# Kernel optimization log

Measured on AMD Instinct MI355X. Metric: run time of the kernel, lower is better.

The kernel has to match this reference:

```python
import jax, jax.numpy as jnp
import numpy as np

N_NODES = 40000
N_EDGES = 320000
N_GRAPHS = 64
IN_DIM = 128
HID4 = 256   # hidden_dim * 4
OUT_DIM = 128
LN_EPS = 1e-5


def setup_inputs() -> dict:
    key = jax.random.key(0)
    ks = jax.random.split(key, 12)
    x = jax.random.normal(ks[0], (N_NODES, IN_DIM), dtype=jnp.float32)
    w = jax.random.uniform(ks[1], (N_EDGES, 4), dtype=jnp.float32)
    src = jax.random.randint(ks[2], (N_EDGES,), 0, N_NODES, dtype=jnp.int32)
    dst = jax.random.randint(ks[3], (N_EDGES,), 0, N_NODES, dtype=jnp.int32)
    graph_ids = jnp.sort(jax.random.randint(ks[4], (N_NODES,), 0, N_GRAPHS, dtype=jnp.int32))
    # parameters (no biases on GraphConv / fc1 linear)
    W1 = jax.random.normal(ks[5], (IN_DIM, HID4), dtype=jnp.float32) / np.sqrt(IN_DIM)
    fc1_W = jax.random.normal(ks[6], (IN_DIM, HID4), dtype=jnp.float32) / np.sqrt(IN_DIM)
    ln_gamma = jnp.ones((HID4,), dtype=jnp.float32)
    ln_beta = jnp.zeros((HID4,), dtype=jnp.float32)
    W2 = jax.random.normal(ks[7], (2 * HID4, HID4), dtype=jnp.float32) / np.sqrt(2 * HID4)
    W3 = jax.random.normal(ks[8], (HID4, OUT_DIM), dtype=jnp.float32) / np.sqrt(HID4)
    return {"x": x, "w": w, "W1": W1, "fc1_W": fc1_W, "ln_gamma": ln_gamma,
            "ln_beta": ln_beta, "W2": W2, "W3": W3,
            "src": src, "dst": dst, "graph_ids": graph_ids}


def _graph_conv(feat, src, dst, ew, W, out_inv_sqrt, in_inv_sqrt):
    # DGL GraphConv, norm='both', bias=False, with scalar edge_weight:
    # h = D_out^{-1/2} x ; m_e = w_e * h[src] ; agg = scatter_add(m, dst) ;
    # out = (D_in^{-1/2} agg) @ W
    h = feat * out_inv_sqrt[:, None]
    m = h[src] * ew[:, None]                       # [E, D] messages
    agg = jax.ops.segment_sum(m, dst, num_segments=N_NODES)
    return (agg * in_inv_sqrt[:, None]) @ W


def reference(x, w, W1, fc1_W, ln_gamma, ln_beta, W2, W3, src, dst, graph_ids):
    # unweighted degree normalization (DGL uses structural degrees, clamp(min=1))
    ones_e = jnp.ones((N_EDGES,), dtype=x.dtype)
    out_deg = jnp.maximum(jax.ops.segment_sum(ones_e, src, num_segments=N_NODES), 1.0)
    in_deg = jnp.maximum(jax.ops.segment_sum(ones_e, dst, num_segments=N_NODES), 1.0)
    out_inv = out_deg ** -0.5
    in_inv = in_deg ** -0.5

    ew = jnp.max(w, axis=1)                        # [E]

    x1 = jax.nn.relu(_graph_conv(x, src, dst, ew, W1, out_inv, in_inv))

    # fc1: Linear(no bias) -> LayerNorm(affine) -> ReLU
    f1 = x @ fc1_W
    mu = jnp.mean(f1, axis=-1, keepdims=True)
    var = jnp.mean((f1 - mu) ** 2, axis=-1, keepdims=True)
    f1 = (f1 - mu) * jax.lax.rsqrt(var + LN_EPS) * ln_gamma + ln_beta
    f1 = jax.nn.relu(f1)

    x1f1 = jnp.concatenate([x1, f1], axis=1)       # [N, 512]
    x2 = jax.nn.relu(_graph_conv(x1f1, src, dst, ew, W2, out_inv, in_inv))
    x3 = jax.nn.relu(_graph_conv(x2, src, dst, ew, W3, out_inv, in_inv))

    # dgl.sum_nodes over batched graph, then row-wise L2 normalize
    readout = jax.ops.segment_sum(x3, graph_ids, num_segments=N_GRAPHS)  # [G, OUT_DIM]
    norm = jnp.maximum(jnp.linalg.norm(readout, axis=1, keepdims=True), 1e-12)
    return readout / norm
```

## Files before the change

### kernel.cpp

```cpp
#include <hip/hip_runtime.h>

#define N_NODES 40000
#define M_PAD   40064
#define N_EDGES 320000
#define N_GRAPHS 64
#define IN_DIM 128
#define HID4 256
#define OUT_DIM 128
#define LN_EPS 1e-5f

typedef short  s16x8  __attribute__((ext_vector_type(8)));
typedef __bf16 bf16x8 __attribute__((ext_vector_type(8)));
typedef float  f32x4  __attribute__((ext_vector_type(4)));

__device__ __forceinline__ unsigned short f2b(float f) {
    unsigned int u = __builtin_bit_cast(unsigned int, f);
    u += 0x7fffu + ((u >> 16) & 1u);
    return (unsigned short)(u >> 16);
}
__device__ __forceinline__ float b2f(unsigned short h) {
    unsigned int u = (unsigned int)h << 16;
    return __builtin_bit_cast(float, u);
}

__device__ __forceinline__ void gll16(const unsigned short* g, short* lds_base) {
    __builtin_amdgcn_global_load_lds(
        (const __attribute__((address_space(1))) unsigned int*)g,
        (__attribute__((address_space(3))) unsigned int*)lds_base, 16, 0, 0);
}


#define XN (N_NODES * IN_DIM)
#define WN 229376
#define PREP_TOT (XN + WN + N_EDGES)

__global__ void prep_all(const float* __restrict__ x, const float* __restrict__ W1,
                         const float* __restrict__ fc1, const float* __restrict__ W2,
                         const float* __restrict__ W3, const float* __restrict__ w,
                         const int* __restrict__ src, const int* __restrict__ dst,
                         unsigned short* __restrict__ xb, unsigned short* __restrict__ W1t,
                         unsigned short* __restrict__ fc1t, unsigned short* __restrict__ W2t,
                         unsigned short* __restrict__ W3t, float* __restrict__ ew,
                         int* __restrict__ cnt_out, int* __restrict__ cnt_in) {
    int idx = blockIdx.x * 256 + threadIdx.x;
    if (idx < XN) { xb[idx] = f2b(x[idx]); return; }
    int j = idx - XN;
    if (j < 32768) { int k = j >> 8, n = j & 255; W1t[n * 128 + k] = f2b(W1[j]); return; }
    j -= 32768;
    if (j < 32768) { int k = j >> 8, n = j & 255; fc1t[n * 128 + k] = f2b(fc1[j]); return; }
    j -= 32768;
    if (j < 131072) { int k = j >> 8, n = j & 255; W2t[n * 512 + k] = f2b(W2[j]); return; }
    j -= 131072;
    if (j < 32768) { int k = j >> 7, n = j & 127; W3t[n * 256 + k] = f2b(W3[j]); return; }
    j -= 32768;
    if (j < N_EDGES) {
        float4 v = ((const float4*)w)[j];
        ew[j] = fmaxf(fmaxf(v.x, v.y), fmaxf(v.z, v.w));
        atomicAdd(&cnt_out[src[j]], 1);
        atomicAdd(&cnt_in[dst[j]], 1);
    }
}

__global__ void scan_part(const int* __restrict__ cnt, int* __restrict__ partial) {
    int b = blockIdx.x;
    int s = 0;
    for (int i = threadIdx.x; i < 1000; i += 256) s += cnt[b * 1000 + i];
#pragma unroll
    for (int m = 1; m < 64; m <<= 1) s += __shfl_xor(s, m);
    __shared__ int wsm[4];
    if ((threadIdx.x & 63) == 0) wsm[threadIdx.x >> 6] = s;
    __syncthreads();
    if (threadIdx.x == 0) partial[b] = wsm[0] + wsm[1] + wsm[2] + wsm[3];
}

__global__ void scan_final(const int* __restrict__ cnt_in, const int* __restrict__ cnt_out,
                           const int* __restrict__ partial, int* __restrict__ off,
                           float* __restrict__ out_inv, float* __restrict__ in_inv) {
    int b = blockIdx.x, tid = threadIdx.x;
    int lane = tid & 63, wv = tid >> 6;
    int pre = 0;
    for (int j = 0; j < b; ++j) pre += partial[j];
    int i = b * 1000 + tid;
    int v = (tid < 1000) ? cnt_in[i] : 0;
    int x = v;
#pragma unroll
    for (int ofs = 1; ofs < 64; ofs <<= 1) {
        int t = __shfl_up(x, ofs);
        if (lane >= ofs) x += t;
    }
    __shared__ int wsum[16];
    if (lane == 63) wsum[wv] = x;
    __syncthreads();
    if (wv == 0 && lane < 16) {
        int s = wsum[lane];
#pragma unroll
        for (int ofs = 1; ofs < 16; ofs <<= 1) {
            int t = __shfl_up(s, ofs);
            if (lane >= ofs) s += t;
        }
        wsum[lane] = s;
    }
    __syncthreads();
    int incl = pre + (wv > 0 ? wsum[wv - 1] : 0) + x;
    if (tid < 1000) {
        off[i] = incl - v;
        in_inv[i] = rsqrtf(fmaxf((float)v, 1.0f));
        out_inv[i] = rsqrtf(fmaxf((float)cnt_out[i], 1.0f));
    }
    if (b == 39 && tid == 999) off[N_NODES] = incl;
}

__global__ void csr_fill(const int* __restrict__ src, const int* __restrict__ dst,
                         const float* __restrict__ ew, const float* __restrict__ out_inv,
                         const int* __restrict__ off, int* __restrict__ cnt_in,
                         int2* __restrict__ es1, int2* __restrict__ es23) {
    int e = blockIdx.x * 256 + threadIdx.x;
    if (e >= N_EDGES) return;
    int d = dst[e];
    int slot = off[d] + atomicSub(&cnt_in[d], 1) - 1;
    int s = src[e];
    float wv = ew[e];
    es1[slot] = make_int2(s, __float_as_int(wv * out_inv[s]));
    es23[slot] = make_int2(s, __float_as_int(wv));
}


template <int D, int RELU>
__global__ void gather_nodes(const unsigned short* __restrict__ h, const int* __restrict__ off,
                             const int2* __restrict__ eg, const float* __restrict__ scale,
                             unsigned short* __restrict__ outb) {
    int n = blockIdx.x;
    int t = threadIdx.x;
    int b = off[n], e = off[n + 1];
    const unsigned int* hu = (const unsigned int*)h;
    float a0 = 0.0f, a1 = 0.0f;
    int i = b;
    for (; i + 3 < e; i += 4) {
        int2 e0 = eg[i], e1 = eg[i + 1], e2 = eg[i + 2], e3 = eg[i + 3];
        unsigned int p0 = hu[(size_t)e0.x * (D / 2) + t];
        unsigned int p1 = hu[(size_t)e1.x * (D / 2) + t];
        unsigned int p2 = hu[(size_t)e2.x * (D / 2) + t];
        unsigned int p3 = hu[(size_t)e3.x * (D / 2) + t];
        float w0 = __int_as_float(e0.y), w1 = __int_as_float(e1.y);
        float w2 = __int_as_float(e2.y), w3 = __int_as_float(e3.y);
        a0 += w0 * b2f((unsigned short)p0) + w1 * b2f((unsigned short)p1)
            + w2 * b2f((unsigned short)p2) + w3 * b2f((unsigned short)p3);
        a1 += w0 * b2f((unsigned short)(p0 >> 16)) + w1 * b2f((unsigned short)(p1 >> 16))
            + w2 * b2f((unsigned short)(p2 >> 16)) + w3 * b2f((unsigned short)(p3 >> 16));
    }
    for (; i < e; ++i) {
        int2 ee = eg[i];
        unsigned int p = hu[(size_t)ee.x * (D / 2) + t];
        float w0 = __int_as_float(ee.y);
        a0 += w0 * b2f((unsigned short)p);
        a1 += w0 * b2f((unsigned short)(p >> 16));
    }
    float sc = scale[n];
    a0 *= sc; a1 *= sc;
    if (RELU) { a0 = fmaxf(a0, 0.0f); a1 = fmaxf(a1, 0.0f); }
    unsigned int o = (unsigned int)f2b(a0) | ((unsigned int)f2b(a1) << 16);
    ((unsigned int*)outb)[(size_t)n * (D / 2) + t] = o;
}


#define G3_NPB 8

__global__ void gather3_ro(const unsigned short* __restrict__ h, const int* __restrict__ off,
                           const int2* __restrict__ eg, const float* __restrict__ scale,
                           const int* __restrict__ gid, float* __restrict__ ro) {
    int t = threadIdx.x;
    int n0 = blockIdx.x * G3_NPB;
    int n1 = n0 + G3_NPB;
    if (n1 > N_NODES) n1 = N_NODES;
    const unsigned int* hu = (const unsigned int*)h;
    float r0 = 0.0f, r1 = 0.0f;
    int cur = gid[n0];
    for (int n = n0; n < n1; ++n) {
        int g = gid[n];
        if (g != cur) {
            atomicAdd(&ro[cur * OUT_DIM + 2 * t], r0);
            atomicAdd(&ro[cur * OUT_DIM + 2 * t + 1], r1);
            r0 = r1 = 0.0f;
            cur = g;
        }
        int b = off[n], e = off[n + 1];
        float a0 = 0.0f, a1 = 0.0f;
        int i = b;
        for (; i + 3 < e; i += 4) {
            int2 e0 = eg[i], e1 = eg[i + 1], e2 = eg[i + 2], e3 = eg[i + 3];
            unsigned int p0 = hu[(size_t)e0.x * 64 + t];
            unsigned int p1 = hu[(size_t)e1.x * 64 + t];
            unsigned int p2 = hu[(size_t)e2.x * 64 + t];
            unsigned int p3 = hu[(size_t)e3.x * 64 + t];
            float w0 = __int_as_float(e0.y), w1 = __int_as_float(e1.y);
            float w2 = __int_as_float(e2.y), w3 = __int_as_float(e3.y);
            a0 += w0 * b2f((unsigned short)p0) + w1 * b2f((unsigned short)p1)
                + w2 * b2f((unsigned short)p2) + w3 * b2f((unsigned short)p3);
            a1 += w0 * b2f((unsigned short)(p0 >> 16)) + w1 * b2f((unsigned short)(p1 >> 16))
                + w2 * b2f((unsigned short)(p2 >> 16)) + w3 * b2f((unsigned short)(p3 >> 16));
        }
        for (; i < e; ++i) {
            int2 ee = eg[i];
            unsigned int p = hu[(size_t)ee.x * 64 + t];
            float w0 = __int_as_float(ee.y);
            a0 += w0 * b2f((unsigned short)p);
            a1 += w0 * b2f((unsigned short)(p >> 16));
        }
        float sc = scale[n];
        r0 += fmaxf(a0 * sc, 0.0f);
        r1 += fmaxf(a1 * sc, 0.0f);
    }
    atomicAdd(&ro[cur * OUT_DIM + 2 * t], r0);
    atomicAdd(&ro[cur * OUT_DIM + 2 * t + 1], r1);
}


__device__ __forceinline__ void gemm_core(short* As, short* Bs,
    const unsigned short* __restrict__ A, const unsigned short* __restrict__ A2,
    const unsigned short* __restrict__ Bt, unsigned short* __restrict__ C,
    const float* __restrict__ rowScaleC, int K1, int K2, int N,
    int relu, int scaleC, int m0, int n0) {
    int tid = threadIdx.x;
    int lane = tid & 63, wave = tid >> 6;
    int wm = (wave >> 1) * 64, wn = (wave & 1) * 64;
    int quad = lane >> 4, r16 = lane & 15;
    const int K = K1 + K2;
    f32x4 acc[4][4] = {};
    int lrow = wave * 16 + (lane >> 2);
    int kc = (lane & 3) * 8;
    short* ldsA = As + wave * 512;
    short* ldsB = Bs + wave * 512;

    for (int k0 = 0; k0 < K; k0 += 32) {
        int kk = k0 + kc;
#pragma unroll
        for (int h = 0; h < 2; ++h) {
            int r = h * 64 + lrow;
            const unsigned short* Ap = (kk < K1)
                ? A  + (size_t)(m0 + r) * K1 + kk
                : A2 + (size_t)(m0 + r) * K2 + (kk - K1);
            gll16(Ap, ldsA + h * 2048);
            gll16(Bt + (size_t)(n0 + r) * K + kk, ldsB + h * 2048);
        }
        __syncthreads();
        s16x8 af[4], bfr[4];
#pragma unroll
        for (int i = 0; i < 4; ++i)
            af[i] = *(const s16x8*)(As + (wm + i * 16 + r16) * 32 + quad * 8);
#pragma unroll
        for (int j = 0; j < 4; ++j)
            bfr[j] = *(const s16x8*)(Bs + (wn + j * 16 + r16) * 32 + quad * 8);
#pragma unroll
        for (int i = 0; i < 4; ++i)
#pragma unroll
            for (int j = 0; j < 4; ++j)
                acc[i][j] = __builtin_amdgcn_mfma_f32_16x16x32_bf16(
                    __builtin_bit_cast(bf16x8, af[i]), __builtin_bit_cast(bf16x8, bfr[j]),
                    acc[i][j], 0, 0, 0);
        __syncthreads();
    }

#pragma unroll
    for (int i = 0; i < 4; ++i) {
        int mbase = m0 + wm + i * 16 + quad * 4;
#pragma unroll
        for (int r = 0; r < 4; ++r) {
            int m = mbase + r;
            float sc = scaleC ? rowScaleC[m] : 1.0f;
#pragma unroll
            for (int j = 0; j < 4; ++j) {
                float v = acc[i][j][r] * sc;
                if (relu) v = fmaxf(v, 0.0f);
                C[(size_t)m * N + n0 + wn + j * 16 + r16] = f2b(v);
            }
        }
    }
}

template <int RELU, int SCALE_C>
__global__ __launch_bounds__(256) void gemm_mfma(
    const unsigned short* __restrict__ A, const unsigned short* __restrict__ A2,
    const unsigned short* __restrict__ Bt, unsigned short* __restrict__ C,
    const float* __restrict__ rowScaleC, int K1, int K2, int N) {
    __shared__ short As[4096];
    __shared__ short Bs[4096];
    gemm_core(As, Bs, A, A2, Bt, C, rowScaleC, K1, K2, N, RELU, SCALE_C,
              blockIdx.x * 128, blockIdx.y * 128);
}


__global__ __launch_bounds__(512) void gemm_dual(
    const unsigned short* __restrict__ A0, const unsigned short* __restrict__ B0,
    unsigned short* __restrict__ C0,
    const unsigned short* __restrict__ A1, const unsigned short* __restrict__ B1,
    unsigned short* __restrict__ C1,
    const float* __restrict__ gamma, const float* __restrict__ beta) {
    __shared__ short As[4096];
    __shared__ short Bs[8192];
    __shared__ float lns[128][4];
    __shared__ float lnq[128][4];
    const unsigned short* A  = blockIdx.z ? A1 : A0;
    const unsigned short* Bt = blockIdx.z ? B1 : B0;
    unsigned short* C        = blockIdx.z ? C1 : C0;
    int tid = threadIdx.x;
    int lane = tid & 63, wave = tid >> 6;
    int wm = (wave >> 2) * 64, wn = (wave & 3) * 64;
    int quad = lane >> 4, r16 = lane & 15;
    int m0 = blockIdx.x * 128;
    f32x4 acc[4][4] = {};
    int lrow = lane >> 2;
    int kc = (lane & 3) * 8;
    short* ldsA = As + wave * 512;
    short* ldsB = Bs + wave * 512;

    for (int k0 = 0; k0 < 128; k0 += 32) {
        int kk = k0 + kc;
        int rr = wave * 16 + lrow;
        gll16(A + (size_t)(m0 + rr) * 128 + kk, ldsA);
        gll16(Bt + (size_t)rr * 128 + kk, ldsB);
        gll16(Bt + (size_t)(128 + rr) * 128 + kk, ldsB + 4096);
        __syncthreads();
        s16x8 af[4], bfr[4];
#pragma unroll
        for (int i = 0; i < 4; ++i)
            af[i] = *(const s16x8*)(As + (wm + i * 16 + r16) * 32 + quad * 8);
#pragma unroll
        for (int j = 0; j < 4; ++j)
            bfr[j] = *(const s16x8*)(Bs + (wn + j * 16 + r16) * 32 + quad * 8);
#pragma unroll
        for (int i = 0; i < 4; ++i)
#pragma unroll
            for (int j = 0; j < 4; ++j)
                acc[i][j] = __builtin_amdgcn_mfma_f32_16x16x32_bf16(
                    __builtin_bit_cast(bf16x8, af[i]), __builtin_bit_cast(bf16x8, bfr[j]),
                    acc[i][j], 0, 0, 0);
        __syncthreads();
    }

    if (blockIdx.z == 0) {
#pragma unroll
        for (int i = 0; i < 4; ++i) {
            int mbase = m0 + wm + i * 16 + quad * 4;
#pragma unroll
            for (int r = 0; r < 4; ++r) {
                int m = mbase + r;
#pragma unroll
                for (int j = 0; j < 4; ++j)
                    C[(size_t)m * 256 + wn + j * 16 + r16] = f2b(fmaxf(acc[i][j][r], 0.0f));
            }
        }
    } else {
#pragma unroll
        for (int i = 0; i < 4; ++i)
#pragma unroll
            for (int r = 0; r < 4; ++r) {
                float s = 0.0f, q = 0.0f;
#pragma unroll
                for (int j = 0; j < 4; ++j) { float v = acc[i][j][r]; s += v; q += v * v; }
#pragma unroll
                for (int m = 1; m < 16; m <<= 1) { s += __shfl_xor(s, m); q += __shfl_xor(q, m); }
                if (r16 == 0) {
                    int row = wm + i * 16 + quad * 4 + r;
                    lns[row][wave & 3] = s;
                    lnq[row][wave & 3] = q;
                }
            }
        __syncthreads();
#pragma unroll
        for (int i = 0; i < 4; ++i) {
#pragma unroll
            for (int r = 0; r < 4; ++r) {
                int row = wm + i * 16 + quad * 4 + r;
                float s = lns[row][0] + lns[row][1] + lns[row][2] + lns[row][3];
                float q = lnq[row][0] + lnq[row][1] + lnq[row][2] + lnq[row][3];
                float mu = s * (1.0f / HID4);
                float var = q * (1.0f / HID4) - mu * mu;
                float rs = rsqrtf(var + LN_EPS);
                int m = m0 + row;
#pragma unroll
                for (int j = 0; j < 4; ++j) {
                    int col = wn + j * 16 + r16;
                    float v = (acc[i][j][r] - mu) * rs * gamma[col] + beta[col];
                    C[(size_t)m * 256 + col] = f2b(fmaxf(v, 0.0f));
                }
            }
        }
    }
}


__global__ void normalize_out(const float* __restrict__ ro, float* __restrict__ out) {
    int g = blockIdx.x;
    int d = threadIdx.x;
    float v = ro[g * OUT_DIM + d];
    float ss = v * v;
#pragma unroll
    for (int m = 1; m < 64; m <<= 1) ss += __shfl_xor(ss, m);
    __shared__ float s2[2];
    if ((d & 63) == 0) s2[d >> 6] = ss;
    __syncthreads();
    float tot = s2[0] + s2[1];
    float norm = fmaxf(sqrtf(tot), 1e-12f);
    out[g * OUT_DIM + d] = v / norm;
}


extern "C" void kernel_launch(void* const* d_in, const int* in_sizes, int n_in,
                              void* d_out, int out_size, void* d_ws, size_t ws_size,
                              hipStream_t stream) {
    const float* x    = (const float*)d_in[0];
    const float* w    = (const float*)d_in[1];
    const float* W1   = (const float*)d_in[2];
    const float* fc1W = (const float*)d_in[3];
    const float* gam  = (const float*)d_in[4];
    const float* bet  = (const float*)d_in[5];
    const float* W2   = (const float*)d_in[6];
    const float* W3   = (const float*)d_in[7];
    const int* src = (const int*)d_in[8];
    const int* dst = (const int*)d_in[9];
    const int* gid = (const int*)d_in[10];
    float* out = (float*)d_out;

    float* ws = (float*)d_ws;
    float* out_inv = ws + 0;
    float* in_inv  = ws + 40000;
    float* ew      = ws + 80000;
    int*   cnt_out = (int*)(ws + 400000);
    int*   cnt_in  = (int*)(ws + 440000);
    float* ro      = ws + 480000;
    unsigned short* W1t  = (unsigned short*)(ws + 488192);
    unsigned short* fc1t = (unsigned short*)(ws + 504576);
    unsigned short* W2t  = (unsigned short*)(ws + 520960);
    unsigned short* W3t  = (unsigned short*)(ws + 586496);
    int*   partial = (int*)(ws + 602880);
    int*   off     = (int*)(ws + 602920);
    int2*  es1     = (int2*)(ws + 642922);
    int2*  es23    = (int2*)(ws + 1282922);
    unsigned short* xb    = (unsigned short*)(ws + 1923000);
    unsigned short* Q3b   = xb;
    unsigned short* agg1b = (unsigned short*)(ws + 4487100);
    unsigned short* x2b   = agg1b;
    unsigned short* x1b   = (unsigned short*)(ws + 9615300);
    unsigned short* f1b   = (unsigned short*)(ws + 14743500);
    unsigned short* P2b   = (unsigned short*)(ws + 19871700);

    hipMemsetAsync(cnt_out, 0, (2 * 40000 + N_GRAPHS * OUT_DIM) * sizeof(float), stream);

    prep_all<<<(PREP_TOT + 255) / 256, 256, 0, stream>>>(x, W1, fc1W, W2, W3, w, src, dst,
                                                         xb, W1t, fc1t, W2t, W3t, ew,
                                                         cnt_out, cnt_in);
    scan_part<<<40, 256, 0, stream>>>(cnt_in, partial);
    scan_final<<<40, 1024, 0, stream>>>(cnt_in, cnt_out, partial, off, out_inv, in_inv);
    csr_fill<<<(N_EDGES + 255) / 256, 256, 0, stream>>>(src, dst, ew, out_inv, off, cnt_in,
                                                        es1, es23);

    gather_nodes<IN_DIM, 0><<<N_NODES, IN_DIM / 2, 0, stream>>>(xb, off, es1, in_inv, agg1b);
    {
        dim3 grid(M_PAD / 128, 1, 2);
        gemm_dual<<<grid, 512, 0, stream>>>(agg1b, W1t, x1b, xb, fc1t, f1b, gam, bet);
    }

    {
        dim3 grid(M_PAD / 128, HID4 / 128);
        gemm_mfma<0, 1><<<grid, 256, 0, stream>>>(x1b, f1b, W2t, P2b, out_inv,
                                                  HID4, HID4, HID4);
    }
    gather_nodes<HID4, 1><<<N_NODES, HID4 / 2, 0, stream>>>(P2b, off, es23, in_inv, x2b);

    {
        dim3 grid(M_PAD / 128, OUT_DIM / 128);
        gemm_mfma<0, 1><<<grid, 256, 0, stream>>>(x2b, nullptr, W3t, Q3b, out_inv,
                                                  HID4, 0, OUT_DIM);
    }
    gather3_ro<<<(N_NODES + G3_NPB - 1) / G3_NPB, 64, 0, stream>>>(Q3b, off, es23, in_inv,
                                                                   gid, ro);
    normalize_out<<<N_GRAPHS, 128, 0, stream>>>(ro, out);
}
```

Measured before the change: 287.5 us.

## Merge edge arrays, widen gather loads, and use BK=64 swizzled LDS GEMM tiles

The two CSR edge arrays are merged into one int4 record holding source, normalized weight and raw weight. The gather kernels now use 64-lane blocks with 8-byte loads per lane. For 128-wide features, the two half-waves handle alternate edges and their sums are combined with a shuffle. The GEMM core moves to a K-step of 64 with an XOR-swizzled LDS layout and doubled shared memory, to cut bank conflicts and barrier count at the cost of more LDS per block (lower occupancy).

Measured after the change: 285.0 us. No clear change (-0.9%).

```diff
diff --git a/kernel.cpp b/kernel.cpp
--- a/kernel.cpp
+++ b/kernel.cpp
@@ -21,6 +21,11 @@
 __device__ __forceinline__ float b2f(unsigned short h) {
     unsigned int u = (unsigned int)h << 16;
     return __builtin_bit_cast(float, u);
+}
+__device__ __forceinline__ float lo2f(unsigned int u) { return b2f((unsigned short)u); }
+__device__ __forceinline__ float hi2f(unsigned int u) { return b2f((unsigned short)(u >> 16)); }
+__device__ __forceinline__ unsigned int packb(float x, float y) {
+    return (unsigned int)f2b(x) | ((unsigned int)f2b(y) << 16);
 }
 
 __device__ __forceinline__ void gll16(const unsigned short* g, short* lds_base) {
@@ -113,105 +118,150 @@
 __global__ void csr_fill(const int* __restrict__ src, const int* __restrict__ dst,
                          const float* __restrict__ ew, const float* __restrict__ out_inv,
                          const int* __restrict__ off, int* __restrict__ cnt_in,
-                         int2* __restrict__ es1, int2* __restrict__ es23) {
+                         int4* __restrict__ es) {
     int e = blockIdx.x * 256 + threadIdx.x;
     if (e >= N_EDGES) return;
     int d = dst[e];
     int slot = off[d] + atomicSub(&cnt_in[d], 1) - 1;
     int s = src[e];
     float wv = ew[e];
-    es1[slot] = make_int2(s, __float_as_int(wv * out_inv[s]));
-    es23[slot] = make_int2(s, __float_as_int(wv));
-}
-
-
-template <int D, int RELU>
+    es[slot] = make_int4(s, __float_as_int(wv * out_inv[s]), __float_as_int(wv), 0);
+}
+
+
+template <int D, int RELU, int WSEL>
 __global__ void gather_nodes(const unsigned short* __restrict__ h, const int* __restrict__ off,
-                             const int2* __restrict__ eg, const float* __restrict__ scale,
+                             const int4* __restrict__ eg, const float* __restrict__ scale,
                              unsigned short* __restrict__ outb) {
     int n = blockIdx.x;
-    int t = threadIdx.x;
+    int lane = threadIdx.x;
     int b = off[n], e = off[n + 1];
-    const unsigned int* hu = (const unsigned int*)h;
-    float a0 = 0.0f, a1 = 0.0f;
-    int i = b;
-    for (; i + 3 < e; i += 4) {
-        int2 e0 = eg[i], e1 = eg[i + 1], e2 = eg[i + 2], e3 = eg[i + 3];
-        unsigned int p0 = hu[(size_t)e0.x * (D / 2) + t];
-        unsigned int p1 = hu[(size_t)e1.x * (D / 2) + t];
-        unsigned int p2 = hu[(size_t)e2.x * (D / 2) + t];
-        unsigned int p3 = hu[(size_t)e3.x * (D / 2) + t];
-        float w0 = __int_as_float(e0.y), w1 = __int_as_float(e1.y);
-        float w2 = __int_as_float(e2.y), w3 = __int_as_float(e3.y);
-        a0 += w0 * b2f((unsigned short)p0) + w1 * b2f((unsigned short)p1)
-            + w2 * b2f((unsigned short)p2) + w3 * b2f((unsigned short)p3);
-        a1 += w0 * b2f((unsigned short)(p0 >> 16)) + w1 * b2f((unsigned short)(p1 >> 16))
-            + w2 * b2f((unsigned short)(p2 >> 16)) + w3 * b2f((unsigned short)(p3 >> 16));
-    }
-    for (; i < e; ++i) {
-        int2 ee = eg[i];
-        unsigned int p = hu[(size_t)ee.x * (D / 2) + t];
-        float w0 = __int_as_float(ee.y);
-        a0 += w0 * b2f((unsigned short)p);
-        a1 += w0 * b2f((unsigned short)(p >> 16));
-    }
-    float sc = scale[n];
-    a0 *= sc; a1 *= sc;
-    if (RELU) { a0 = fmaxf(a0, 0.0f); a1 = fmaxf(a1, 0.0f); }
-    unsigned int o = (unsigned int)f2b(a0) | ((unsigned int)f2b(a1) << 16);
-    ((unsigned int*)outb)[(size_t)n * (D / 2) + t] = o;
+    const uint2* hu = (const uint2*)h;
+    float a0 = 0.f, a1 = 0.f, a2 = 0.f, a3 = 0.f;
+    if constexpr (D == 256) {
+        int i = b;
+        for (; i + 3 < e; i += 4) {
+            int4 e0 = eg[i], e1 = eg[i + 1], e2 = eg[i + 2], e3 = eg[i + 3];
+            uint2 p0 = hu[(size_t)e0.x * 64 + lane];
+            uint2 p1 = hu[(size_t)e1.x * 64 + lane];
+            uint2 p2 = hu[(size_t)e2.x * 64 + lane];
+            uint2 p3 = hu[(size_t)e3.x * 64 + lane];
+            float w0 = __int_as_float(WSEL ? e0.z : e0.y);
+            float w1 = __int_as_float(WSEL ? e1.z : e1.y);
+            float w2 = __int_as_float(WSEL ? e2.z : e2.y);
+            float w3 = __int_as_float(WSEL ? e3.z : e3.y);
+            a0 += w0 * lo2f(p0.x) + w1 * lo2f(p1.x) + w2 * lo2f(p2.x) + w3 * lo2f(p3.x);
+            a1 += w0 * hi2f(p0.x) + w1 * hi2f(p1.x) + w2 * hi2f(p2.x) + w3 * hi2f(p3.x);
+            a2 += w0 * lo2f(p0.y) + w1 * lo2f(p1.y) + w2 * lo2f(p2.y) + w3 * lo2f(p3.y);
+            a3 += w0 * hi2f(p0.y) + w1 * hi2f(p1.y) + w2 * hi2f(p2.y) + w3 * hi2f(p3.y);
+        }
+        for (; i < e; ++i) {
+            int4 ee = eg[i];
+            uint2 p = hu[(size_t)ee.x * 64 + lane];
+            float w0 = __int_as_float(WSEL ? ee.z : ee.y);
+            a0 += w0 * lo2f(p.x); a1 += w0 * hi2f(p.x);
+            a2 += w0 * lo2f(p.y); a3 += w0 * hi2f(p.y);
+        }
+        float sc = scale[n];
+        a0 *= sc; a1 *= sc; a2 *= sc; a3 *= sc;
+        if (RELU) {
+            a0 = fmaxf(a0, 0.f); a1 = fmaxf(a1, 0.f);
+            a2 = fmaxf(a2, 0.f); a3 = fmaxf(a3, 0.f);
+        }
+        uint2 o; o.x = packb(a0, a1); o.y = packb(a2, a3);
+        ((uint2*)outb)[(size_t)n * 64 + lane] = o;
+    } else {
+        int half = lane >> 5, cl = lane & 31;
+        int i = b;
+        for (; i + 3 < e; i += 4) {
+            int4 ea = eg[i + half];
+            int4 eb = eg[i + 2 + half];
+            uint2 pa = hu[(size_t)ea.x * 32 + cl];
+            uint2 pb = hu[(size_t)eb.x * 32 + cl];
+            float wa = __int_as_float(WSEL ? ea.z : ea.y);
+            float wb = __int_as_float(WSEL ? eb.z : eb.y);
+            a0 += wa * lo2f(pa.x) + wb * lo2f(pb.x);
+            a1 += wa * hi2f(pa.x) + wb * hi2f(pb.x);
+            a2 += wa * lo2f(pa.y) + wb * lo2f(pb.y);
+            a3 += wa * hi2f(pa.y) + wb * hi2f(pb.y);
+        }
+        for (; i < e; i += 2) {
+            int idx = i + half;
+            int4 ee = eg[idx < e ? idx : i];
+            float w = (idx < e) ? __int_as_float(WSEL ? ee.z : ee.y) : 0.0f;
+            uint2 p = hu[(size_t)ee.x * 32 + cl];
+            a0 += w * lo2f(p.x); a1 += w * hi2f(p.x);
+            a2 += w * lo2f(p.y); a3 += w * hi2f(p.y);
+        }
+        a0 += __shfl_xor(a0, 32); a1 += __shfl_xor(a1, 32);
+        a2 += __shfl_xor(a2, 32); a3 += __shfl_xor(a3, 32);
+        float sc = scale[n];
+        a0 *= sc; a1 *= sc; a2 *= sc; a3 *= sc;
+        if (RELU) {
+            a0 = fmaxf(a0, 0.f); a1 = fmaxf(a1, 0.f);
+            a2 = fmaxf(a2, 0.f); a3 = fmaxf(a3, 0.f);
+        }
+        if (half == 0) {
+            uint2 o; o.x = packb(a0, a1); o.y = packb(a2, a3);
+            ((uint2*)outb)[(size_t)n * 32 + cl] = o;
+        }
+    }
 }
 
 
 #define G3_NPB 8
 
 __global__ void gather3_ro(const unsigned short* __restrict__ h, const int* __restrict__ off,
-                           const int2* __restrict__ eg, const float* __restrict__ scale,
+                           const int4* __restrict__ eg, const float* __restrict__ scale,
                            const int* __restrict__ gid, float* __restrict__ ro) {
-    int t = threadIdx.x;
+    int lane = threadIdx.x;
+    int half = lane >> 5, cl = lane & 31;
     int n0 = blockIdx.x * G3_NPB;
     int n1 = n0 + G3_NPB;
     if (n1 > N_NODES) n1 = N_NODES;
-    const unsigned int* hu = (const unsigned int*)h;
-    float r0 = 0.0f, r1 = 0.0f;
+    const uint2* hu = (const uint2*)h;
+    float r0 = 0.f, r1 = 0.f, r2 = 0.f, r3 = 0.f;
     int cur = gid[n0];
     for (int n = n0; n < n1; ++n) {
         int g = gid[n];
         if (g != cur) {
-            atomicAdd(&ro[cur * OUT_DIM + 2 * t], r0);
-            atomicAdd(&ro[cur * OUT_DIM + 2 * t + 1], r1);
-            r0 = r1 = 0.0f;
+            atomicAdd(&ro[cur * OUT_DIM + 4 * cl + 2 * half], half ? r2 : r0);
+            atomicAdd(&ro[cur * OUT_DIM + 4 * cl + 2 * half + 1], half ? r3 : r1);
+            r0 = r1 = r2 = r3 = 0.f;
             cur = g;
         }
         int b = off[n], e = off[n + 1];
-        float a0 = 0.0f, a1 = 0.0f;
+        float a0 = 0.f, a1 = 0.f, a2 = 0.f, a3 = 0.f;
         int i = b;
         for (; i + 3 < e; i += 4) {
-            int2 e0 = eg[i], e1 = eg[i + 1], e2 = eg[i + 2], e3 = eg[i + 3];
-            unsigned int p0 = hu[(size_t)e0.x * 64 + t];
-            unsigned int p1 = hu[(size_t)e1.x * 64 + t];
-            unsigned int p2 = hu[(size_t)e2.x * 64 + t];
-            unsigned int p3 = hu[(size_t)e3.x * 64 + t];
-            float w0 = __int_as_float(e0.y), w1 = __int_as_float(e1.y);
-            float w2 = __int_as_float(e2.y), w3 = __int_as_float(e3.y);
-            a0 += w0 * b2f((unsigned short)p0) + w1 * b2f((unsigned short)p1)
-                + w2 * b2f((unsigned short)p2) + w3 * b2f((unsigned short)p3);
-            a1 += w0 * b2f((unsigned short)(p0 >> 16)) + w1 * b2f((unsigned short)(p1 >> 16))
-                + w2 * b2f((unsigned short)(p2 >> 16)) + w3 * b2f((unsigned short)(p3 >> 16));
-        }
-        for (; i < e; ++i) {
-            int2 ee = eg[i];
-            unsigned int p = hu[(size_t)ee.x * 64 + t];
-            float w0 = __int_as_float(ee.y);
-            a0 += w0 * b2f((unsigned short)p);
-            a1 += w0 * b2f((unsigned short)(p >> 16));
-        }
+            int4 ea = eg[i + half];
+            int4 eb = eg[i + 2 + half];
+            uint2 pa = hu[(size_t)ea.x * 32 + cl];
+            uint2 pb = hu[(size_t)eb.x * 32 + cl];
+            float wa = __int_as_float(ea.z), wb = __int_as_float(eb.z);
+            a0 += wa * lo2f(pa.x) + wb * lo2f(pb.x);
+            a1 += wa * hi2f(pa.x) + wb * hi2f(pb.x);
+            a2 += wa * lo2f(pa.y) + wb * lo2f(pb.y);
+            a3 += wa * hi2f(pa.y) + wb * hi2f(pb.y);
+        }
+        for (; i < e; i += 2) {
+            int idx = i + half;
+            int4 ee = eg[idx < e ? idx : i];
+            float w = (idx < e) ? __int_as_float(ee.z) : 0.0f;
+            uint2 p = hu[(size_t)ee.x * 32 + cl];
+            a0 += w * lo2f(p.x); a1 += w * hi2f(p.x);
+            a2 += w * lo2f(p.y); a3 += w * hi2f(p.y);
+        }
+        a0 += __shfl_xor(a0, 32); a1 += __shfl_xor(a1, 32);
+        a2 += __shfl_xor(a2, 32); a3 += __shfl_xor(a3, 32);
         float sc = scale[n];
         r0 += fmaxf(a0 * sc, 0.0f);
         r1 += fmaxf(a1 * sc, 0.0f);
-    }
-    atomicAdd(&ro[cur * OUT_DIM + 2 * t], r0);
-    atomicAdd(&ro[cur * OUT_DIM + 2 * t + 1], r1);
+        r2 += fmaxf(a2 * sc, 0.0f);
+        r3 += fmaxf(a3 * sc, 0.0f);
+    }
+    atomicAdd(&ro[cur * OUT_DIM + 4 * cl + 2 * half], half ? r2 : r0);
+    atomicAdd(&ro[cur * OUT_DIM + 4 * cl + 2 * half + 1], half ? r3 : r1);
 }
 
 
@@ -226,37 +276,42 @@
     int quad = lane >> 4, r16 = lane & 15;
     const int K = K1 + K2;
     f32x4 acc[4][4] = {};
-    int lrow = wave * 16 + (lane >> 2);
-    int kc = (lane & 3) * 8;
-    short* ldsA = As + wave * 512;
-    short* ldsB = Bs + wave * 512;
-
-    for (int k0 = 0; k0 < K; k0 += 32) {
-        int kk = k0 + kc;
-#pragma unroll
-        for (int h = 0; h < 2; ++h) {
-            int r = h * 64 + lrow;
-            const unsigned short* Ap = (kk < K1)
+    int srow = lane >> 3;
+    int sk   = ((lane & 7) ^ srow) * 8;
+    int xorc = r16 & 7;
+    short* ldsA = As + wave * 2048;
+    short* ldsB = Bs + wave * 2048;
+
+    for (int k0 = 0; k0 < K; k0 += 64) {
+        int kk = k0 + sk;
+#pragma unroll
+        for (int h = 0; h < 4; ++h) {
+            int r = wave * 32 + h * 8 + srow;
+            const unsigned short* Ap = (k0 < K1)
                 ? A  + (size_t)(m0 + r) * K1 + kk
                 : A2 + (size_t)(m0 + r) * K2 + (kk - K1);
-            gll16(Ap, ldsA + h * 2048);
-            gll16(Bt + (size_t)(n0 + r) * K + kk, ldsB + h * 2048);
+            gll16(Ap, ldsA + h * 512);
+            gll16(Bt + (size_t)(n0 + r) * K + kk, ldsB + h * 512);
         }
         __syncthreads();
-        s16x8 af[4], bfr[4];
-#pragma unroll
-        for (int i = 0; i < 4; ++i)
-            af[i] = *(const s16x8*)(As + (wm + i * 16 + r16) * 32 + quad * 8);
-#pragma unroll
-        for (int j = 0; j < 4; ++j)
-            bfr[j] = *(const s16x8*)(Bs + (wn + j * 16 + r16) * 32 + quad * 8);
-#pragma unroll
-        for (int i = 0; i < 4; ++i)
+#pragma unroll
+        for (int c = 0; c < 2; ++c) {
+            s16x8 af[4], bfr[4];
+            int pc = (((c * 4 + quad) ^ xorc) << 3);
+#pragma unroll
+            for (int i = 0; i < 4; ++i)
+                af[i] = *(const s16x8*)(As + (wm + i * 16 + r16) * 64 + pc);
 #pragma unroll
             for (int j = 0; j < 4; ++j)
-                acc[i][j] = __builtin_amdgcn_mfma_f32_16x16x32_bf16(
-                    __builtin_bit_cast(bf16x8, af[i]), __builtin_bit_cast(bf16x8, bfr[j]),
-                    acc[i][j], 0, 0, 0);
+                bfr[j] = *(const s16x8*)(Bs + (wn + j * 16 + r16) * 64 + pc);
+#pragma unroll
+            for (int i = 0; i < 4; ++i)
+#pragma unroll
+                for (int j = 0; j < 4; ++j)
+                    acc[i][j] = __builtin_amdgcn_mfma_f32_16x16x32_bf16(
+                        __builtin_bit_cast(bf16x8, af[i]), __builtin_bit_cast(bf16x8, bfr[j]),
+                        acc[i][j], 0, 0, 0);
+        }
         __syncthreads();
     }
 
@@ -282,8 +337,8 @@
     const unsigned short* __restrict__ A, const unsigned short* __restrict__ A2,
     const unsigned short* __restrict__ Bt, unsigned short* __restrict__ C,
     const float* __restrict__ rowScaleC, int K1, int K2, int N) {
-    __shared__ short As[4096];
-    __shared__ short Bs[4096];
+    __shared__ short As[8192];
+    __shared__ short Bs[8192];
     gemm_core(As, Bs, A, A2, Bt, C, rowScaleC, K1, K2, N, RELU, SCALE_C,
               blockIdx.x * 128, blockIdx.y * 128);
 }
@@ -434,8 +489,7 @@
     unsigned short* W3t  = (unsigned short*)(ws + 586496);
     int*   partial = (int*)(ws + 602880);
     int*   off     = (int*)(ws + 602920);
-    int2*  es1     = (int2*)(ws + 642922);
-    int2*  es23    = (int2*)(ws + 1282922);
+    int4*  es      = (int4*)(ws + 642924);
     unsigned short* xb    = (unsigned short*)(ws + 1923000);
     unsigned short* Q3b   = xb;
     unsigned short* agg1b = (unsigned short*)(ws + 4487100);
@@ -451,10 +505,9 @@
                                                          cnt_out, cnt_in);
     scan_part<<<40, 256, 0, stream>>>(cnt_in, partial);
     scan_final<<<40, 1024, 0, stream>>>(cnt_in, cnt_out, partial, off, out_inv, in_inv);
-    csr_fill<<<(N_EDGES + 255) / 256, 256, 0, stream>>>(src, dst, ew, out_inv, off, cnt_in,
-                                                        es1, es23);
-
-    gather_nodes<IN_DIM, 0><<<N_NODES, IN_DIM / 2, 0, stream>>>(xb, off, es1, in_inv, agg1b);
+    csr_fill<<<(N_EDGES + 255) / 256, 256, 0, stream>>>(src, dst, ew, out_inv, off, cnt_in, es);
+
+    gather_nodes<IN_DIM, 0, 0><<<N_NODES, 64, 0, stream>>>(xb, off, es, in_inv, agg1b);
     {
         dim3 grid(M_PAD / 128, 1, 2);
         gemm_dual<<<grid, 512, 0, stream>>>(agg1b, W1t, x1b, xb, fc1t, f1b, gam, bet);
@@ -465,14 +518,14 @@
         gemm_mfma<0, 1><<<grid, 256, 0, stream>>>(x1b, f1b, W2t, P2b, out_inv,
                                                   HID4, HID4, HID4);
     }
-    gather_nodes<HID4, 1><<<N_NODES, HID4 / 2, 0, stream>>>(P2b, off, es23, in_inv, x2b);
+    gather_nodes<HID4, 1, 1><<<N_NODES, 64, 0, stream>>>(P2b, off, es, in_inv, x2b);
 
     {
         dim3 grid(M_PAD / 128, OUT_DIM / 128);
         gemm_mfma<0, 1><<<grid, 256, 0, stream>>>(x2b, nullptr, W3t, Q3b, out_inv,
                                                   HID4, 0, OUT_DIM);
     }
-    gather3_ro<<<(N_NODES + G3_NPB - 1) / G3_NPB, 64, 0, stream>>>(Q3b, off, es23, in_inv,
+    gather3_ro<<<(N_NODES + G3_NPB - 1) / G3_NPB, 64, 0, stream>>>(Q3b, off, es, in_inv,
                                                                    gid, ro);
     normalize_out<<<N_GRAPHS, 128, 0, stream>>>(ro, out);
 }
```
